# Optimization experiments

Hardware: AMD Instinct MI355X
Metric: run time of the kernel (lower is better)

The kernel has to match this reference:

```python
import jax, jax.numpy as jnp
import numpy as np

B, T, D, H, C = 32, 160, 512, 256, 6625  # batch, time, feat, gru hidden, num classes


def _gru_scan(x_proj, rk, rbias):
    """Keras GRU (reset_after=True) over time.
    x_proj: [T, B, 3H] = x @ kernel + input_bias (precomputed).
    rk: [H, 3H] recurrent kernel, rbias: [3H] recurrent bias.
    Returns hidden states [T, B, H]."""
    h0 = jnp.zeros((x_proj.shape[1], rk.shape[0]), dtype=x_proj.dtype)

    def step(h, xp):
        inner = h @ rk + rbias                 # [B, 3H]
        xz, xr, xh = jnp.split(xp, 3, axis=-1)
        rz, rr, rh = jnp.split(inner, 3, axis=-1)
        z = jax.nn.sigmoid(xz + rz)            # update gate
        r = jax.nn.sigmoid(xr + rr)            # reset gate
        hh = jnp.tanh(xh + r * rh)             # candidate
        hn = z * h + (1.0 - z) * hh
        return hn, hn

    _, hs = jax.lax.scan(step, h0, x_proj)
    return hs  # [T, B, H]


def setup_inputs() -> dict:
    key = jax.random.key(0)
    ks = jax.random.split(key, 9)
    s_in, s_rec, s_cls = 1.0 / np.sqrt(D), 1.0 / np.sqrt(H), 0.1
    return {
        "x": jax.random.normal(ks[0], (B, T, D), jnp.float32),
        "kernel_fwd": jax.random.normal(ks[1], (D, 3 * H), jnp.float32) * s_in,
        "rk_fwd": jax.random.normal(ks[2], (H, 3 * H), jnp.float32) * s_rec,
        "bias_fwd": jnp.zeros((2, 3 * H), jnp.float32),
        "kernel_bwd": jax.random.normal(ks[3], (D, 3 * H), jnp.float32) * s_in,
        "rk_bwd": jax.random.normal(ks[4], (H, 3 * H), jnp.float32) * s_rec,
        "bias_bwd": jnp.zeros((2, 3 * H), jnp.float32),
        "W": jax.random.truncated_normal(ks[5], -2.0, 2.0, (2 * H, C), jnp.float32) * s_cls,
        "b": jnp.zeros((C,), jnp.float32),
    }


def reference(x, kernel_fwd, rk_fwd, bias_fwd, kernel_bwd, rk_bwd, bias_bwd, W, b):
    x_t = jnp.transpose(x, (1, 0, 2))                       # [T, B, D]
    # forward direction
    xp_f = x_t @ kernel_fwd + bias_fwd[0]                   # [T, B, 3H]
    h_f = _gru_scan(xp_f, rk_fwd, bias_fwd[1])              # [T, B, H]
    # backward direction: run on time-reversed input, reverse output
    x_rev = x_t[::-1]
    xp_b = x_rev @ kernel_bwd + bias_bwd[0]
    h_b = _gru_scan(xp_b, rk_bwd, bias_bwd[1])[::-1]        # [T, B, H]
    out = jnp.concatenate([h_f, h_b], axis=-1)              # [T, B, 2H]
    # classifier applied per position; original reshape/matmul/reshape/transpose
    # ([B,T,2H]->[-1,2H]@W -> [B,T,C] -> [T,B,C]) is equivalent to this:
    logits = out @ W + b                                    # [T, B, C]
    return logits
```

## Files before the change

### kernel.cpp

```cpp
#include <hip/hip_runtime.h>
#include <hip/hip_bf16.h>


#define B 32
#define T 160
#define D 512
#define H 256
#define C 6625
#define H3 768
#define NT16 416
#define KP_PER_DIR 393216

typedef __attribute__((ext_vector_type(8))) short short8v;
typedef __attribute__((ext_vector_type(4))) float float4v;

__device__ inline unsigned short f2bf(float v) {
    __hip_bfloat16 b = __float2bfloat16(v);
    return *reinterpret_cast<unsigned short*>(&b);
}
__device__ inline float bflo(unsigned int u) { return __uint_as_float(u << 16); }
__device__ inline float bfhi(unsigned int u) { return __uint_as_float(u & 0xffff0000u); }

#if __has_builtin(__builtin_amdgcn_fdot2_f32_bf16)
#define HAVE_DOT2 1
typedef __attribute__((ext_vector_type(2))) __bf16 bf16x2v;
__device__ inline float dot2bf(unsigned int w, unsigned int h, float acc) {
    return __builtin_amdgcn_fdot2_f32_bf16(
        __builtin_bit_cast(bf16x2v, w), __builtin_bit_cast(bf16x2v, h), acc, false);
}
#else
#define HAVE_DOT2 0
#endif

__global__ __launch_bounds__(256) void pack_rkT_kernel(
    const float* __restrict__ rkf, const float* __restrict__ rkb,
    unsigned int* __restrict__ rkT)
{
    const int idx = blockIdx.x * 256 + threadIdx.x;
    const int j   = idx & 255;
    const int p   = (idx >> 8) & 127;
    const int g   = (idx >> 15) % 3;
    const int dir = idx / (3 << 15);
    const float* rk = dir ? rkb : rkf;
    const int col = g * 256 + j;
    unsigned int lo = f2bf(rk[(2 * p) * H3 + col]);
    unsigned int hi = f2bf(rk[(2 * p + 1) * H3 + col]);
    rkT[idx] = (hi << 16) | lo;
}

__global__ __launch_bounds__(256) void pack_W_kernel(
    const float* __restrict__ W, unsigned short* __restrict__ Wp)
{
    const int idx = blockIdx.x * 256 + threadIdx.x;
    const int i   = idx & 7;
    const int col = (idx >> 3) & 15;
    const int kc  = (idx >> 7) & 63;
    const int nt  = idx >> 13;
    const int k = kc * 8 + i;
    const int c = nt * 16 + col;
    const float v = (c < C) ? W[k * C + c] : 0.f;
    Wp[idx] = f2bf(v);
}

__global__ __launch_bounds__(256) void pack_xb_kernel(
    const float* __restrict__ x, unsigned short* __restrict__ xb)
{
    const int idx = blockIdx.x * 256 + threadIdx.x;
    const int k   = idx & 511;
    const int row = idx >> 9;
    const int t   = row >> 5;
    const int b   = row & 31;
    xb[idx] = f2bf(x[(b * T + t) * 512 + k]);
}

__global__ __launch_bounds__(256) void pack_kern_kernel(
    const float* __restrict__ kf, const float* __restrict__ kb,
    unsigned short* __restrict__ kernP)
{
    const int idx = blockIdx.x * 256 + threadIdx.x;
    const int dir = blockIdx.y;
    const float* kern = dir ? kb : kf;
    const int i   = idx & 7;
    const int col = (idx >> 3) & 15;
    const int kc  = (idx >> 7) & 63;
    const int nt  = idx >> 13;
    kernP[dir * KP_PER_DIR + idx] = f2bf(kern[(kc * 8 + i) * H3 + nt * 16 + col]);
}

__global__ __launch_bounds__(256) void proj_mfma_kernel(
    const unsigned short* __restrict__ xb,
    const unsigned short* __restrict__ kernP,
    const float* __restrict__ bias_f,
    const float* __restrict__ bias_b,
    float* __restrict__ xp)
{
    const int bid = blockIdx.x;
    const int ct  = bid / 40;
    const int rt  = bid % 40;
    const int dir = blockIdx.y;
    const int lane = threadIdx.x & 63;
    const int wid  = threadIdx.x >> 6;
    const int wm = wid >> 1, wn = wid & 1;
    const int rowBase = rt * 128 + wm * 64;
    const int lrow = lane & 15;
    const int lk8  = lane >> 4;
    const float* bias = dir ? bias_b : bias_f;

    float4v acc[4][4];
#pragma unroll
    for (int i = 0; i < 4; ++i)
#pragma unroll
        for (int k = 0; k < 4; ++k) acc[i][k] = (float4v){0.f, 0.f, 0.f, 0.f};

    const short* A  = (const short*)xb;
    const short* Bp = (const short*)(kernP + dir * KP_PER_DIR);
    const int ntBase = ct * 8 + wn * 4;

    int arow[4];
#pragma unroll
    for (int mt = 0; mt < 4; ++mt) {
        const int r0 = rowBase + mt * 16;
        const int s  = r0 >> 5;
        arow[mt] = (dir ? (159 - s) : s) * 32 + (r0 & 31);
    }

    for (int k0 = 0; k0 < 512; k0 += 32) {
        short8v aF[4], bF[4];
#pragma unroll
        for (int mt = 0; mt < 4; ++mt)
            aF[mt] = *(const short8v*)&A[(arow[mt] + lrow) * 512 + k0 + lk8 * 8];
#pragma unroll
        for (int ntw = 0; ntw < 4; ++ntw)
            bF[ntw] = *(const short8v*)&Bp[((ntBase + ntw) * 64 + (k0 >> 3) + lk8) * 128 + lrow * 8];
#pragma unroll
        for (int mt = 0; mt < 4; ++mt)
#pragma unroll
            for (int ntw = 0; ntw < 4; ++ntw)
                acc[mt][ntw] = __builtin_amdgcn_mfma_f32_16x16x32_bf16(
                    aF[mt], bF[ntw], acc[mt][ntw], 0, 0, 0);
    }

    const int orow = (lane >> 4) * 4;
#pragma unroll
    for (int ntw = 0; ntw < 4; ++ntw) {
        const int c = (ntBase + ntw) * 16 + lrow;
        const float bc = bias[c];
#pragma unroll
        for (int mt = 0; mt < 4; ++mt)
#pragma unroll
            for (int v = 0; v < 4; ++v)
                xp[(size_t)(dir * 5120 + rowBase + mt * 16 + orow + v) * H3 + c]
                    = acc[mt][ntw][v] + bc;
    }
}

__global__ __launch_bounds__(768, 3) void gru_scan_v5(
    const float* __restrict__ xp,
    const unsigned int* __restrict__ rkT,
    const float* __restrict__ bias_f,
    const float* __restrict__ bias_b,
    __hip_bfloat16* __restrict__ hcatb)
{
    const int bid = blockIdx.x;
    const int dir = bid >> 5;
    const int b   = bid & 31;
    const int tid = threadIdx.x;
    const int g   = tid >> 8;
    const int j   = tid & 255;
    const float* bias = dir ? bias_b : bias_f;

    const unsigned int* wsrc = rkT + ((dir * 3 + g) << 15) + j;
    unsigned int w[128];
#pragma unroll
    for (int p = 0; p < 128; ++p) w[p] = wsrc[p << 8];

    float rbz = 0.f, rbr = 0.f, rbh = 0.f;
    if (tid < 256) {
        rbz = bias[H3 + j];
        rbr = bias[H3 + 256 + j];
        rbh = bias[H3 + 512 + j];
    }

    __shared__ float hfp[256];
    __shared__ unsigned int hbf[128];
    __shared__ float sums[2][256];
    if (tid < 256) hfp[tid] = 0.f;
    if (tid < 128) hbf[tid] = 0u;
    __syncthreads();

    for (int s = 0; s < T; ++s) {
        float xz = 0.f, xr = 0.f, xh = 0.f;
        if (tid < 256) {
            const float* xrow = xp + ((dir * T + s) * B + b) * H3;
            xz = xrow[j];
            xr = xrow[256 + j];
            xh = xrow[512 + j];
        }

        float a0 = 0.f, a1 = 0.f, a2 = 0.f, a3 = 0.f;
#if HAVE_DOT2
        {
            const uint4* h4 = (const uint4*)hbf;
#pragma unroll
            for (int q = 0; q < 32; ++q) {
                uint4 hv = h4[q];
                a0 = dot2bf(w[4 * q + 0], hv.x, a0);
                a1 = dot2bf(w[4 * q + 1], hv.y, a1);
                a2 = dot2bf(w[4 * q + 2], hv.z, a2);
                a3 = dot2bf(w[4 * q + 3], hv.w, a3);
                if ((q & 7) == 7) __builtin_amdgcn_sched_barrier(0);
            }
        }
#else
#pragma unroll
        for (int q = 0; q < 32; ++q) {
            float4 h01 = *(const float4*)&hfp[8 * q];
            float4 h23 = *(const float4*)&hfp[8 * q + 4];
            a0 += h01.x * bflo(w[4 * q + 0]) + h01.y * bfhi(w[4 * q + 0]);
            a1 += h01.z * bflo(w[4 * q + 1]) + h01.w * bfhi(w[4 * q + 1]);
            a2 += h23.x * bflo(w[4 * q + 2]) + h23.y * bfhi(w[4 * q + 2]);
            a3 += h23.z * bflo(w[4 * q + 3]) + h23.w * bfhi(w[4 * q + 3]);
            if ((q & 7) == 7) __builtin_amdgcn_sched_barrier(0);
        }
#endif
        const float dot = (a0 + a1) + (a2 + a3);
        if (g > 0) sums[g - 1][j] = dot;
        __syncthreads();

        if (tid < 256) {
            const float sz = dot;
            const float sr = sums[0][j];
            const float sh = sums[1][j];
            const float z  = 1.f / (1.f + __expf(-(xz + sz + rbz)));
            const float r  = 1.f / (1.f + __expf(-(xr + sr + rbr)));
            const float pre = xh + r * (sh + rbh);
            const float e2  = __expf(2.f * pre);
            const float hh  = 1.f - 2.f / (e2 + 1.f);
            const float hn  = z * hfp[j] + (1.f - z) * hh;
            hfp[j] = hn;
#if HAVE_DOT2
            ((unsigned short*)hbf)[j] = f2bf(hn);
#endif
            const int ta = dir ? (T - 1 - s) : s;
            hcatb[(ta * B + b) * 512 + dir * 256 + j] = __float2bfloat16(hn);
        }
        __syncthreads();
    }
}

__global__ __launch_bounds__(256) void cls_mfma_kernel(
    const __hip_bfloat16* __restrict__ hcatb,
    const unsigned short* __restrict__ Wp,
    const float* __restrict__ bias,
    float* __restrict__ out)
{
    const int bid = blockIdx.x;
    const int ct  = bid / 40;
    const int rt  = bid % 40;
    const int lane = threadIdx.x & 63;
    const int wid  = threadIdx.x >> 6;
    const int wm = wid >> 1, wn = wid & 1;
    const int rowBase = rt * 128 + wm * 64;
    const int lrow = lane & 15;
    const int lk8  = lane >> 4;

    float4v acc[4][4];
#pragma unroll
    for (int i = 0; i < 4; ++i)
#pragma unroll
        for (int k = 0; k < 4; ++k) acc[i][k] = (float4v){0.f, 0.f, 0.f, 0.f};

    const short* A  = (const short*)hcatb;
    const short* Bp = (const short*)Wp;
    const int ntBase = ct * 8 + wn * 4;

    for (int k0 = 0; k0 < 512; k0 += 32) {
        short8v aF[4], bF[4];
#pragma unroll
        for (int mt = 0; mt < 4; ++mt)
            aF[mt] = *(const short8v*)&A[(rowBase + mt * 16 + lrow) * 512 + k0 + lk8 * 8];
#pragma unroll
        for (int ntw = 0; ntw < 4; ++ntw)
            bF[ntw] = *(const short8v*)&Bp[((ntBase + ntw) * 64 + (k0 >> 3) + lk8) * 128 + lrow * 8];
#pragma unroll
        for (int mt = 0; mt < 4; ++mt)
#pragma unroll
            for (int ntw = 0; ntw < 4; ++ntw)
                acc[mt][ntw] = __builtin_amdgcn_mfma_f32_16x16x32_bf16(
                    aF[mt], bF[ntw], acc[mt][ntw], 0, 0, 0);
    }

    const int orow = (lane >> 4) * 4;
#pragma unroll
    for (int ntw = 0; ntw < 4; ++ntw) {
        const int c = (ntBase + ntw) * 16 + lrow;
        if (c >= C) continue;
        const float bc = bias[c];
#pragma unroll
        for (int mt = 0; mt < 4; ++mt)
#pragma unroll
            for (int v = 0; v < 4; ++v)
                out[(size_t)(rowBase + mt * 16 + orow + v) * C + c] = acc[mt][ntw][v] + bc;
    }
}

__global__ __launch_bounds__(256) void proj_kernel(
    const float* __restrict__ x, const float* __restrict__ kf,
    const float* __restrict__ kb, const float* __restrict__ bias_f,
    const float* __restrict__ bias_b, float* __restrict__ xp)
{
    const int ct  = blockIdx.x;
    const int s   = blockIdx.y;
    const int dir = blockIdx.z;
    const int tid = threadIdx.x;
    const int t   = dir ? (T - 1 - s) : s;
    const float* kern = dir ? kb : kf;
    const float* bias = dir ? bias_b : bias_f;

    __shared__ float xs[32 * 512];
    for (int it = 0; it < 16; ++it) {
        int v = it * 256 + tid, row = v >> 7, k4 = v & 127;
        *(float4*)&xs[(row << 9) + (k4 << 2)] =
            *(const float4*)&x[((row * T + t) << 9) + (k4 << 2)];
    }
    __syncthreads();

    const int col = ct * 256 + tid;
    float acc[32];
#pragma unroll
    for (int r = 0; r < 32; ++r) acc[r] = 0.f;
    for (int k = 0; k < 512; k += 4) {
        float w0 = kern[(k + 0) * H3 + col];
        float w1 = kern[(k + 1) * H3 + col];
        float w2 = kern[(k + 2) * H3 + col];
        float w3 = kern[(k + 3) * H3 + col];
#pragma unroll
        for (int r = 0; r < 32; ++r) {
            float4 xv = *(const float4*)&xs[(r << 9) + k];
            acc[r] += xv.x * w0 + xv.y * w1 + xv.z * w2 + xv.w * w3;
        }
    }
    const float bb = bias[col];
    for (int r = 0; r < 32; ++r)
        xp[((dir * T + s) * B + r) * H3 + col] = acc[r] + bb;
}

__global__ __launch_bounds__(1024) void gru_scan_f32(
    const float* __restrict__ xp,
    const float* __restrict__ rk_f, const float* __restrict__ rk_b,
    const float* __restrict__ bias_f, const float* __restrict__ bias_b,
    float* __restrict__ hcat)
{
    const int bid = blockIdx.x;
    const int dir = bid >> 5;
    const int b   = bid & 31;
    const int tid = threadIdx.x;
    const int kg  = tid >> 8;
    const int j   = tid & 255;
    const int k0  = kg << 6;
    const float* rk   = dir ? rk_b : rk_f;
    const float* bias = dir ? bias_b : bias_f;
    const float rbz = bias[H3 + j];
    const float rbr = bias[H3 + 256 + j];
    const float rbh = bias[H3 + 512 + j];

    __shared__ float h[256];
    __shared__ float part[3][4][256];
    if (tid < 256) h[tid] = 0.f;
    __syncthreads();

    for (int s = 0; s < T; ++s) {
        const float* xrow = xp + ((dir * T + s) * B + b) * H3;
        float az = 0.f, ar = 0.f, ah = 0.f;
#pragma unroll 4
        for (int k = k0; k < k0 + 64; k += 4) {
            float4 h4 = *(const float4*)&h[k];
            const float* rkp = rk + k * H3 + j;
            az += h4.x * rkp[0];       ar += h4.x * rkp[256];       ah += h4.x * rkp[512];
            az += h4.y * rkp[H3];      ar += h4.y * rkp[H3+256];    ah += h4.y * rkp[H3+512];
            az += h4.z * rkp[2*H3];    ar += h4.z * rkp[2*H3+256];  ah += h4.z * rkp[2*H3+512];
            az += h4.w * rkp[3*H3];    ar += h4.w * rkp[3*H3+256];  ah += h4.w * rkp[3*H3+512];
        }
        part[0][kg][j] = az; part[1][kg][j] = ar; part[2][kg][j] = ah;
        __syncthreads();
        if (tid < 256) {
            const float sz = part[0][0][tid]+part[0][1][tid]+part[0][2][tid]+part[0][3][tid];
            const float sr = part[1][0][tid]+part[1][1][tid]+part[1][2][tid]+part[1][3][tid];
            const float sh = part[2][0][tid]+part[2][1][tid]+part[2][2][tid]+part[2][3][tid];
            const float xz = xrow[tid], xr = xrow[256+tid], xh = xrow[512+tid];
            const float z  = 1.f / (1.f + __expf(-(xz + sz + rbz)));
            const float r  = 1.f / (1.f + __expf(-(xr + sr + rbr)));
            const float pre = xh + r * (sh + rbh);
            const float e2  = __expf(2.f * pre);
            const float hh  = 1.f - 2.f / (e2 + 1.f);
            const float hn  = z * h[tid] + (1.f - z) * hh;
            h[tid] = hn;
            const int ta = dir ? (T - 1 - s) : s;
            hcat[(ta * B + b) * (2 * H) + dir * H + tid] = hn;
        }
        __syncthreads();
    }
}

__global__ __launch_bounds__(256) void cls_f32_kernel(
    const float* __restrict__ hcat, const float* __restrict__ W,
    const float* __restrict__ bias, float* __restrict__ out)
{
    const int bid = blockIdx.x;
    const int ct  = bid / 160;
    const int rt  = bid % 160;
    const int tid = threadIdx.x;
    const int r0  = rt * 32;

    __shared__ float hs[32 * 512];
    for (int it = 0; it < 16; ++it) {
        int v = it * 256 + tid, row = v >> 7, k4 = v & 127;
        *(float4*)&hs[(row << 9) + (k4 << 2)] =
            *(const float4*)&hcat[((r0 + row) << 9) + (k4 << 2)];
    }
    __syncthreads();

    const int c0 = ct * 512 + tid;
    const int c1 = c0 + 256;
    const bool v1 = (c1 < C);
    float acc0[32], acc1[32];
#pragma unroll
    for (int r = 0; r < 32; ++r) { acc0[r] = 0.f; acc1[r] = 0.f; }
    for (int k = 0; k < 512; k += 4) {
        const float* wp = W + k * C;
        float w00 = wp[c0], w01 = wp[C+c0], w02 = wp[2*C+c0], w03 = wp[3*C+c0];
        float w10 = v1 ? wp[c1] : 0.f, w11 = v1 ? wp[C+c1] : 0.f;
        float w12 = v1 ? wp[2*C+c1] : 0.f, w13 = v1 ? wp[3*C+c1] : 0.f;
#pragma unroll
        for (int r = 0; r < 32; ++r) {
            float4 hv = *(const float4*)&hs[(r << 9) + k];
            acc0[r] += hv.x*w00 + hv.y*w01 + hv.z*w02 + hv.w*w03;
            acc1[r] += hv.x*w10 + hv.y*w11 + hv.z*w12 + hv.w*w13;
        }
    }
    const float b0 = bias[c0];
    const float b1 = v1 ? bias[c1] : 0.f;
    for (int r = 0; r < 32; ++r) {
        out[(size_t)(r0+r)*C + c0] = acc0[r] + b0;
        if (v1) out[(size_t)(r0+r)*C + c1] = acc1[r] + b1;
    }
}

extern "C" void kernel_launch(void* const* d_in, const int* in_sizes, int n_in,
                              void* d_out, int out_size, void* d_ws, size_t ws_size,
                              hipStream_t stream) {
    const float* x     = (const float*)d_in[0];
    const float* kf    = (const float*)d_in[1];
    const float* rkf   = (const float*)d_in[2];
    const float* biasf = (const float*)d_in[3];
    const float* kb    = (const float*)d_in[4];
    const float* rkb   = (const float*)d_in[5];
    const float* biasb = (const float*)d_in[6];
    const float* W     = (const float*)d_in[7];
    const float* bvec  = (const float*)d_in[8];
    float* out = (float*)d_out;

    const size_t rkT_bytes   = (size_t)2 * 3 * 128 * 256 * 4;
    const size_t Wp_bytes    = (size_t)NT16 * 8192 * 2;
    const size_t hcatb_bytes = (size_t)T * B * 2 * H * 2;
    const size_t planA_bytes = rkT_bytes + Wp_bytes + hcatb_bytes;

    float*          xp    = out;
    unsigned short* xb    = (unsigned short*)((char*)out + (size_t)2 * 5120 * H3 * 4);
    unsigned short* kernP = (unsigned short*)((char*)xb + (size_t)5120 * 512 * 2);

    if (ws_size >= planA_bytes) {
        char* wsb = (char*)d_ws;
        unsigned int*   rkT   = (unsigned int*)wsb;
        unsigned short* Wp    = (unsigned short*)(wsb + rkT_bytes);
        __hip_bfloat16* hcatb = (__hip_bfloat16*)(wsb + rkT_bytes + Wp_bytes);

        pack_rkT_kernel<<<768, 256, 0, stream>>>(rkf, rkb, rkT);
        pack_W_kernel<<<13312, 256, 0, stream>>>(W, Wp);
        pack_xb_kernel<<<10240, 256, 0, stream>>>(x, xb);
        pack_kern_kernel<<<dim3(1536, 2), 256, 0, stream>>>(kf, kb, kernP);

        proj_mfma_kernel<<<dim3(240, 2), 256, 0, stream>>>(xb, kernP, biasf, biasb, xp);

        gru_scan_v5<<<64, 768, 0, stream>>>(xp, rkT, biasf, biasb, hcatb);

        cls_mfma_kernel<<<2080, 256, 0, stream>>>(hcatb, Wp, bvec, out);
    } else {
        float* hcat = (float*)d_ws;
        dim3 g1(3, T, 2);
        proj_kernel<<<g1, 256, 0, stream>>>(x, kf, kb, biasf, biasb, xp);
        gru_scan_f32<<<64, 1024, 0, stream>>>(xp, rkf, rkb, biasf, biasb, hcat);
        cls_f32_kernel<<<13 * 160, 256, 0, stream>>>(hcat, W, bvec, out);
    }
}
```

Measured before the change: 362.3 us.

## Compute GRU recurrent matvec with bf16 MFMA instead of dot2 VALU

Recurrent weights are repacked into the MFMA B-fragment layout, and each of the 12 waves holds 4 column tiles in registers. The per-step h·Rk product now runs as 16x16x32 bf16 MFMAs with h broadcast across all 16 A rows, replacing 128 fdot2 VALU instructions per thread. Row 0 of each tile is written to shared memory for the gate stage. This moves the serial per-step math onto the matrix units and cuts LDS reads, but 15 of the 16 MFMA rows are wasted and each accumulator has a chain of 8 dependent MFMAs, which adds latency.

After: 336.9 us. 7.0% less time.

```diff
diff --git a/kernel.cpp b/kernel.cpp
--- a/kernel.cpp
+++ b/kernel.cpp
@@ -10,6 +10,7 @@
 #define H3 768
 #define NT16 416
 #define KP_PER_DIR 393216
+#define RKB_PER_DIR 196608
 
 typedef __attribute__((ext_vector_type(8))) short short8v;
 typedef __attribute__((ext_vector_type(4))) float float4v;
@@ -18,34 +19,19 @@
     __hip_bfloat16 b = __float2bfloat16(v);
     return *reinterpret_cast<unsigned short*>(&b);
 }
-__device__ inline float bflo(unsigned int u) { return __uint_as_float(u << 16); }
-__device__ inline float bfhi(unsigned int u) { return __uint_as_float(u & 0xffff0000u); }
-
-#if __has_builtin(__builtin_amdgcn_fdot2_f32_bf16)
-#define HAVE_DOT2 1
-typedef __attribute__((ext_vector_type(2))) __bf16 bf16x2v;
-__device__ inline float dot2bf(unsigned int w, unsigned int h, float acc) {
-    return __builtin_amdgcn_fdot2_f32_bf16(
-        __builtin_bit_cast(bf16x2v, w), __builtin_bit_cast(bf16x2v, h), acc, false);
-}
-#else
-#define HAVE_DOT2 0
-#endif
-
-__global__ __launch_bounds__(256) void pack_rkT_kernel(
+
+__global__ __launch_bounds__(256) void pack_rkB_kernel(
     const float* __restrict__ rkf, const float* __restrict__ rkb,
-    unsigned int* __restrict__ rkT)
+    unsigned short* __restrict__ rkB)
 {
     const int idx = blockIdx.x * 256 + threadIdx.x;
-    const int j   = idx & 255;
-    const int p   = (idx >> 8) & 127;
-    const int g   = (idx >> 15) % 3;
-    const int dir = idx / (3 << 15);
+    const int dir = blockIdx.y;
     const float* rk = dir ? rkb : rkf;
-    const int col = g * 256 + j;
-    unsigned int lo = f2bf(rk[(2 * p) * H3 + col]);
-    unsigned int hi = f2bf(rk[(2 * p + 1) * H3 + col]);
-    rkT[idx] = (hi << 16) | lo;
+    const int i   = idx & 7;
+    const int col = (idx >> 3) & 15;
+    const int kc  = (idx >> 7) & 31;
+    const int nt  = idx >> 12;
+    rkB[dir * RKB_PER_DIR + idx] = f2bf(rk[(kc * 8 + i) * H3 + nt * 16 + col]);
 }
 
 __global__ __launch_bounds__(256) void pack_W_kernel(
@@ -154,9 +140,9 @@
     }
 }
 
-__global__ __launch_bounds__(768, 3) void gru_scan_v5(
+__global__ __launch_bounds__(768, 3) void gru_scan_v6(
     const float* __restrict__ xp,
-    const unsigned int* __restrict__ rkT,
+    const unsigned short* __restrict__ rkB,
     const float* __restrict__ bias_f,
     const float* __restrict__ bias_b,
     __hip_bfloat16* __restrict__ hcatb)
@@ -165,14 +151,21 @@
     const int dir = bid >> 5;
     const int b   = bid & 31;
     const int tid = threadIdx.x;
-    const int g   = tid >> 8;
+    const int wv  = tid >> 6;
+    const int lane = tid & 63;
+    const int lrow = lane & 15;
+    const int lk8  = lane >> 4;
     const int j   = tid & 255;
     const float* bias = dir ? bias_b : bias_f;
-
-    const unsigned int* wsrc = rkT + ((dir * 3 + g) << 15) + j;
-    unsigned int w[128];
-#pragma unroll
-    for (int p = 0; p < 128; ++p) w[p] = wsrc[p << 8];
+    const short* Bp = (const short*)(rkB + (size_t)dir * RKB_PER_DIR);
+
+    short8v bw[32];
+#pragma unroll
+    for (int i = 0; i < 4; ++i)
+#pragma unroll
+        for (int kk = 0; kk < 8; ++kk)
+            bw[i * 8 + kk] = *(const short8v*)
+                &Bp[(((wv * 4 + i) * 32) + kk * 4 + lk8) * 128 + lrow * 8];
 
     float rbz = 0.f, rbr = 0.f, rbh = 0.f;
     if (tid < 256) {
@@ -182,10 +175,9 @@
     }
 
     __shared__ float hfp[256];
-    __shared__ unsigned int hbf[128];
-    __shared__ float sums[2][256];
-    if (tid < 256) hfp[tid] = 0.f;
-    if (tid < 128) hbf[tid] = 0u;
+    __shared__ __align__(16) unsigned short hus[256];
+    __shared__ float sums[768];
+    if (tid < 256) { hfp[tid] = 0.f; hus[tid] = 0; }
     __syncthreads();
 
     for (int s = 0; s < T; ++s) {
@@ -197,40 +189,28 @@
             xh = xrow[512 + j];
         }
 
-        float a0 = 0.f, a1 = 0.f, a2 = 0.f, a3 = 0.f;
-#if HAVE_DOT2
-        {
-            const uint4* h4 = (const uint4*)hbf;
-#pragma unroll
-            for (int q = 0; q < 32; ++q) {
-                uint4 hv = h4[q];
-                a0 = dot2bf(w[4 * q + 0], hv.x, a0);
-                a1 = dot2bf(w[4 * q + 1], hv.y, a1);
-                a2 = dot2bf(w[4 * q + 2], hv.z, a2);
-                a3 = dot2bf(w[4 * q + 3], hv.w, a3);
-                if ((q & 7) == 7) __builtin_amdgcn_sched_barrier(0);
-            }
-        }
-#else
-#pragma unroll
-        for (int q = 0; q < 32; ++q) {
-            float4 h01 = *(const float4*)&hfp[8 * q];
-            float4 h23 = *(const float4*)&hfp[8 * q + 4];
-            a0 += h01.x * bflo(w[4 * q + 0]) + h01.y * bfhi(w[4 * q + 0]);
-            a1 += h01.z * bflo(w[4 * q + 1]) + h01.w * bfhi(w[4 * q + 1]);
-            a2 += h23.x * bflo(w[4 * q + 2]) + h23.y * bfhi(w[4 * q + 2]);
-            a3 += h23.z * bflo(w[4 * q + 3]) + h23.w * bfhi(w[4 * q + 3]);
-            if ((q & 7) == 7) __builtin_amdgcn_sched_barrier(0);
-        }
-#endif
-        const float dot = (a0 + a1) + (a2 + a3);
-        if (g > 0) sums[g - 1][j] = dot;
+        float4v a0 = {0.f,0.f,0.f,0.f}, a1 = {0.f,0.f,0.f,0.f};
+        float4v a2 = {0.f,0.f,0.f,0.f}, a3 = {0.f,0.f,0.f,0.f};
+#pragma unroll
+        for (int kk = 0; kk < 8; ++kk) {
+            short8v aF = *(const short8v*)&hus[kk * 32 + lk8 * 8];
+            a0 = __builtin_amdgcn_mfma_f32_16x16x32_bf16(aF, bw[0 * 8 + kk], a0, 0, 0, 0);
+            a1 = __builtin_amdgcn_mfma_f32_16x16x32_bf16(aF, bw[1 * 8 + kk], a1, 0, 0, 0);
+            a2 = __builtin_amdgcn_mfma_f32_16x16x32_bf16(aF, bw[2 * 8 + kk], a2, 0, 0, 0);
+            a3 = __builtin_amdgcn_mfma_f32_16x16x32_bf16(aF, bw[3 * 8 + kk], a3, 0, 0, 0);
+        }
+        if (lane < 16) {
+            sums[(wv * 4 + 0) * 16 + lane] = a0[0];
+            sums[(wv * 4 + 1) * 16 + lane] = a1[0];
+            sums[(wv * 4 + 2) * 16 + lane] = a2[0];
+            sums[(wv * 4 + 3) * 16 + lane] = a3[0];
+        }
         __syncthreads();
 
         if (tid < 256) {
-            const float sz = dot;
-            const float sr = sums[0][j];
-            const float sh = sums[1][j];
+            const float sz = sums[j];
+            const float sr = sums[256 + j];
+            const float sh = sums[512 + j];
             const float z  = 1.f / (1.f + __expf(-(xz + sz + rbz)));
             const float r  = 1.f / (1.f + __expf(-(xr + sr + rbr)));
             const float pre = xh + r * (sh + rbh);
@@ -238,9 +218,7 @@
             const float hh  = 1.f - 2.f / (e2 + 1.f);
             const float hn  = z * hfp[j] + (1.f - z) * hh;
             hfp[j] = hn;
-#if HAVE_DOT2
-            ((unsigned short*)hbf)[j] = f2bf(hn);
-#endif
+            hus[j] = f2bf(hn);
             const int ta = dir ? (T - 1 - s) : s;
             hcatb[(ta * B + b) * 512 + dir * 256 + j] = __float2bfloat16(hn);
         }
@@ -460,10 +438,10 @@
     const float* bvec  = (const float*)d_in[8];
     float* out = (float*)d_out;
 
-    const size_t rkT_bytes   = (size_t)2 * 3 * 128 * 256 * 4;
+    const size_t rkB_bytes   = (size_t)2 * RKB_PER_DIR * 2;
     const size_t Wp_bytes    = (size_t)NT16 * 8192 * 2;
     const size_t hcatb_bytes = (size_t)T * B * 2 * H * 2;
-    const size_t planA_bytes = rkT_bytes + Wp_bytes + hcatb_bytes;
+    const size_t planA_bytes = rkB_bytes + Wp_bytes + hcatb_bytes;
 
     float*          xp    = out;
     unsigned short* xb    = (unsigned short*)((char*)out + (size_t)2 * 5120 * H3 * 4);
@@ -471,18 +449,18 @@
 
     if (ws_size >= planA_bytes) {
         char* wsb = (char*)d_ws;
-        unsigned int*   rkT   = (unsigned int*)wsb;
-        unsigned short* Wp    = (unsigned short*)(wsb + rkT_bytes);
-        __hip_bfloat16* hcatb = (__hip_bfloat16*)(wsb + rkT_bytes + Wp_bytes);
-
-        pack_rkT_kernel<<<768, 256, 0, stream>>>(rkf, rkb, rkT);
+        unsigned short* rkB   = (unsigned short*)wsb;
+        unsigned short* Wp    = (unsigned short*)(wsb + rkB_bytes);
+        __hip_bfloat16* hcatb = (__hip_bfloat16*)(wsb + rkB_bytes + Wp_bytes);
+
+        pack_rkB_kernel<<<dim3(768, 2), 256, 0, stream>>>(rkf, rkb, rkB);
         pack_W_kernel<<<13312, 256, 0, stream>>>(W, Wp);
         pack_xb_kernel<<<10240, 256, 0, stream>>>(x, xb);
         pack_kern_kernel<<<dim3(1536, 2), 256, 0, stream>>>(kf, kb, kernP);
 
         proj_mfma_kernel<<<dim3(240, 2), 256, 0, stream>>>(xb, kernP, biasf, biasb, xp);
 
-        gru_scan_v5<<<64, 768, 0, stream>>>(xp, rkT, biasf, biasb, hcatb);
+        gru_scan_v6<<<64, 768, 0, stream>>>(xp, rkB, biasf, biasb, hcatb);
 
         cls_mfma_kernel<<<2080, 256, 0, stream>>>(hcatb, Wp, bvec, out);
     } else {
```
